# Performance work log

Measured on AMD Instinct MI355X. Metric: run time of the kernel, lower is better.

Reference implementation:

```python
import jax, jax.numpy as jnp
import numpy as np

EPS = 1e-12  # torch F.normalize eps

def _l2norm(t):
    # normalize over last axis (N), clamp norm like torch.nn.functional.normalize
    n = jnp.linalg.norm(t, axis=-1, keepdims=True)
    return t / jnp.maximum(n, EPS)

def setup_inputs() -> dict:
    key = jax.random.key(0)
    ks = jax.random.split(key, 4)
    B, N, D, H = 8, 4096, 768, 16
    x = jax.random.normal(ks[0], (B, N, D), dtype=jnp.float32)
    w_qkv = jax.random.normal(ks[1], (D, 3 * D), dtype=jnp.float32) * (D ** -0.5)
    temperature = jnp.ones((H, 1, 1), dtype=jnp.float32)
    w_proj = jax.random.normal(ks[2], (D, D), dtype=jnp.float32) * (D ** -0.5)
    b_proj = jnp.zeros((D,), dtype=jnp.float32)
    return {"x": x, "w_qkv": w_qkv, "temperature": temperature,
            "w_proj": w_proj, "b_proj": b_proj}

def reference(x, w_qkv, temperature, w_proj, b_proj):
    B, N, D = x.shape
    H = temperature.shape[0]
    C = D // H
    # qkv linear (no bias), split last dim as (3, H, C), move to (3, B, H, C, N)
    qkv = (x @ w_qkv).reshape(B, N, 3, H, C).transpose(2, 0, 3, 4, 1)
    q, k, v = qkv[0], qkv[1], qkv[2]            # each [B, H, C, N]
    q = _l2norm(q)
    k = _l2norm(k)
    # cross-covariance attention: small CxC matrix per head
    attn = jnp.einsum('bhcn,bhdn->bhcd', q, k) * temperature  # [B,H,C,C]
    attn = jax.nn.softmax(attn, axis=-1)
    out = jnp.einsum('bhcd,bhdn->bhcn', attn, v)  # [B,H,C,N]
    out = out.transpose(0, 3, 1, 2).reshape(B, N, D)  # B N (H C)
    return out @ w_proj + b_proj
```

## Files before the change

kernel.cpp:

```cpp
#include <hip/hip_runtime.h>
#include <stdint.h>

typedef __attribute__((ext_vector_type(4))) float          f32x4;
typedef __attribute__((ext_vector_type(8))) short          bf16x8;
typedef __attribute__((ext_vector_type(8))) unsigned short u16x8;
typedef __attribute__((ext_vector_type(4))) unsigned short u16x4;

static __device__ __forceinline__ unsigned short f2bf(float f){
  uint32_t u = __builtin_bit_cast(uint32_t, f);
  u += 0x7FFFu + ((u >> 16) & 1u);
  return (unsigned short)(u >> 16);
}
static __device__ __forceinline__ float bf2f(unsigned short h){
  uint32_t u = ((uint32_t)h) << 16;
  return __builtin_bit_cast(float, u);
}

static __device__ __forceinline__ uint32_t f2e4m3(float x){
  uint32_t u = __builtin_bit_cast(uint32_t, x);
  uint32_t s = (u >> 24) & 0x80u;
  uint32_t a = u & 0x7FFFFFFFu;
  if (a >= 0x43E00000u) return s | 0x7Eu;
  int ebits = (int)(a >> 23);
  uint32_t mfull = (a & 0x7FFFFFu) | 0x800000u;
  int shift = (ebits >= 121) ? 20 : 20 + (121 - ebits);
  if (shift > 31) return s;
  uint32_t q = mfull >> shift;
  uint32_t rem = mfull & ((1u << shift) - 1u);
  uint32_t half = 1u << (shift - 1);
  q += (rem > half || (rem == half && (q & 1u)));
  if (ebits >= 121){
    uint32_t E = (uint32_t)(ebits - 121 + 1);
    if (q == 16u){ E += 1u; q = 8u; }
    uint32_t man = q - 8u;
    if (E > 15u || (E == 15u && man == 7u)) return s | 0x7Eu;
    return s | (E << 3) | man;
  } else {
    if (q >= 8u) return s | (1u << 3) | (q - 8u);
    return s | q;
  }
}

static __device__ __forceinline__ uint32_t pk4_e4m3(float a0, float a1, float a2, float a3){
#if __has_builtin(__builtin_amdgcn_cvt_pk_fp8_f32)
  uint32_t pk = (uint32_t)__builtin_amdgcn_cvt_pk_fp8_f32(a0, a1, 0, false);
  pk = (uint32_t)__builtin_amdgcn_cvt_pk_fp8_f32(a2, a3, (int)pk, true);
  return pk;
#else
  return f2e4m3(a0) | (f2e4m3(a1) << 8) | (f2e4m3(a2) << 16) | (f2e4m3(a3) << 24);
#endif
}

#define GLL(SRC, DST) __builtin_amdgcn_global_load_lds(                         \
    (const __attribute__((address_space(1))) unsigned int*)(SRC),               \
    (__attribute__((address_space(3))) unsigned int*)(DST), 16, 0, 0)

__global__ void k_cvt(const float* __restrict__ in, unsigned short* __restrict__ out, long n){
  long i = ((long)blockIdx.x * blockDim.x + threadIdx.x) * 8;
  if (i >= n) return;
  const f32x4* p = (const f32x4*)(in + i);
  f32x4 a = p[0], b = p[1];
  u16x8 o;
  #pragma unroll
  for (int j = 0; j < 4; j++){ o[j] = f2bf(a[j]); o[4+j] = f2bf(b[j]); }
  *(u16x8*)(out + i) = o;
}

__global__ void k_tconv2(const float* __restrict__ wqkv, const float* __restrict__ wproj,
                         unsigned short* __restrict__ WT, unsigned short* __restrict__ WpT){
  __shared__ float tl[64][65];
  const int bx = blockIdx.x;
  const float* in = (bx < 24) ? wqkv : wproj;
  unsigned short* out = (bx < 24) ? WT : WpT;
  const int C = (bx < 24) ? 2304 : 768;
  const int c0 = ((bx < 24) ? bx : bx - 24) * 64, r0 = blockIdx.y * 64;
  const int t = threadIdx.x;
  {
    const int lr = t >> 2, lc = (t & 3) * 16;
    const f32x4* s = (const f32x4*)(in + (long)(r0 + lr) * C + c0 + lc);
    #pragma unroll
    for (int q = 0; q < 4; q++){
      f32x4 v = s[q];
      #pragma unroll
      for (int j = 0; j < 4; j++) tl[lr][lc + q*4 + j] = v[j];
    }
  }
  __syncthreads();
  {
    const int oc = t >> 2, orr = (t & 3) * 16;
    u16x8 o0, o1;
    #pragma unroll
    for (int i = 0; i < 8; i++){ o0[i] = f2bf(tl[orr + i][oc]); o1[i] = f2bf(tl[orr + 8 + i][oc]); }
    u16x8* dst = (u16x8*)(out + (long)(c0 + oc) * 768 + r0 + orr);
    dst[0] = o0; dst[1] = o1;
  }
}

__global__ void k_cvtwv(const float* __restrict__ w, unsigned short* __restrict__ out){
  const long idx = ((long)blockIdx.x * blockDim.x + threadIdx.x) * 8;
  const int e = (int)(idx / 768), hd = (int)(idx - (long)e * 768);
  const float* s = w + (long)e * 2304 + 1536 + hd;
  f32x4 a = *(const f32x4*)s, b = *(const f32x4*)(s + 4);
  u16x8 o;
  #pragma unroll
  for (int j = 0; j < 4; j++){ o[j] = f2bf(a[j]); o[4+j] = f2bf(b[j]); }
  *(u16x8*)(out + idx) = o;
}

static __device__ __forceinline__ bf16x8 ldfrag(const char* slot, int row, int ko){
  const int k2 = (ko ^ (row >> 1)) & 3;
  return *(const bf16x8*)(slot + row*64 + k2*16);
}

static __device__ __forceinline__ void stg256(const unsigned short* __restrict__ G, int row0, int ke,
                                              char* lds_slot, int t){
  #pragma unroll
  for (int l = 0; l < 2; l++){
    const int r  = l*128 + (t >> 2);
    const int k2 = (t & 3) ^ ((r >> 1) & 3);
    GLL((const char*)(G + (long)(row0 + r) * 768 + ke + k2 * 8),
        lds_slot + l*8192 + (t & 0x1C0) * 16);
  }
}

#define PHASE(BUF, KK, MH, STAGE_STMT, WAIT_STMT) do {                         \
    bf16x8 af[4];                                                              \
    if (MH == 0) {                                                             \
      _Pragma("unroll")                                                        \
      for (int ni = 0; ni < 4; ni++)                                           \
        bq[ni] = ldfrag(sB[BUF][KK], wn*64 + ni*16 + arow, ko);                \
    }                                                                          \
    _Pragma("unroll")                                                          \
    for (int mi = 0; mi < 4; mi++)                                             \
      af[mi] = ldfrag(sA[BUF][KK], wm*128 + MH*64 + mi*16 + arow, ko);         \
    __builtin_amdgcn_s_barrier();                                              \
    __builtin_amdgcn_s_setprio(1);                                             \
    _Pragma("unroll")                                                          \
    for (int mi = 0; mi < 4; mi++)                                             \
      _Pragma("unroll")                                                        \
      for (int ni = 0; ni < 4; ni++)                                           \
        acc[MH*4+mi][ni] = __builtin_amdgcn_mfma_f32_16x16x32_bf16(            \
            af[mi], bq[ni], acc[MH*4+mi][ni], 0, 0, 0);                        \
    __builtin_amdgcn_s_setprio(0);                                             \
    STAGE_STMT;                                                                \
    WAIT_STMT;                                                                 \
    __builtin_amdgcn_s_barrier();                                              \
  } while(0)

__global__ __launch_bounds__(512, 2)
void k_gemm256(const unsigned short* __restrict__ A, const unsigned short* __restrict__ BT,
               unsigned char* __restrict__ QT8, unsigned char* __restrict__ KT8,
               float* __restrict__ nrmp)
{
  __shared__ __attribute__((aligned(16))) char lds[131072];
  const int o  = blockIdx.x;
  const int wg = (o & 7) * 96 + (o >> 3);
  const int jt = wg % 6, mt = wg / 6;
  const int m0 = mt * 256, j0 = jt * 256;
  const int t = threadIdx.x, lane = t & 63, w = t >> 6;
  const int wm = w >> 2, wn = w & 3;
  const int arow = lane & 15, ko = lane >> 4;

  char* const sA[2][2] = {{lds,           lds + 16384},
                          {lds + 65536,   lds + 65536 + 16384}};
  char* const sB[2][2] = {{lds + 32768,   lds + 49152},
                          {lds + 65536 + 32768, lds + 65536 + 49152}};

  f32x4 acc[8][4] = {};

  stg256(BT, j0, 0,   sB[0][0], t);
  stg256(A,  m0, 0,   sA[0][0], t);
  stg256(BT, j0, 32,  sB[0][1], t);
  stg256(A,  m0, 32,  sA[0][1], t);
  stg256(BT, j0, 64,  sB[1][0], t);
  stg256(A,  m0, 64,  sA[1][0], t);
  stg256(BT, j0, 96,  sB[1][1], t);
  asm volatile("s_waitcnt vmcnt(6)" ::: "memory");
  __builtin_amdgcn_s_barrier();

  #pragma unroll 1
  for (int it = 0; it < 6; ++it){
    const int t1 = 2*it + 1, t2 = 2*it + 2, t3 = 2*it + 3;
    bf16x8 bq[4];
    PHASE(0,0,0, { stg256(A, m0, t1*64+32, sA[1][1], t); }, ;);
    PHASE(0,0,1, { if (t2 < 12) stg256(BT, j0, t2*64,    sB[0][0], t); }, ;);
    PHASE(0,1,0, { if (t2 < 12) stg256(A,  m0, t2*64,    sA[0][0], t); }, ;);
    PHASE(0,1,1, { if (t2 < 12) stg256(BT, j0, t2*64+32, sB[0][1], t); },
                 { if (it == 5) asm volatile("s_waitcnt vmcnt(0)" ::: "memory");
                   else         asm volatile("s_waitcnt vmcnt(6)" ::: "memory"); });
    PHASE(1,0,0, { if (t2 < 12) stg256(A,  m0, t2*64+32, sA[0][1], t); }, ;);
    PHASE(1,0,1, { if (t3 < 12) stg256(BT, j0, t3*64,    sB[1][0], t); }, ;);
    PHASE(1,1,0, { if (t3 < 12) stg256(A,  m0, t3*64,    sA[1][0], t); }, ;);
    PHASE(1,1,1, { if (t3 < 12) stg256(BT, j0, t3*64+32, sB[1][1], t); },
                 { if (it == 5) asm volatile("s_waitcnt vmcnt(0)" ::: "memory");
                   else         asm volatile("s_waitcnt vmcnt(6)" ::: "memory"); });
  }

  const int b = m0 >> 12;
  const int chunk = ((m0 & 4095) >> 7) + wm;
  #pragma unroll
  for (int ni = 0; ni < 4; ni++){
    float ss = 0.f;
    #pragma unroll
    for (int mi = 0; mi < 8; mi++)
      #pragma unroll
      for (int r = 0; r < 4; r++) ss += acc[mi][ni][r] * acc[mi][ni][r];
    ss += __shfl_xor(ss, 16);
    ss += __shfl_xor(ss, 32);
    if (lane < 16){
      const int jc = j0 + wn*64 + ni*16 + lane;
      const int s  = (jc >= 768);
      const int jl = jc - s * 768;
      const int h  = jl / 48;
      const int c  = jl - h * 48;
      nrmp[(long)(s*6144 + (b*16 + h)*48 + c)*32 + chunk] = ss;
    }
  }
  #pragma unroll
  for (int mi = 0; mi < 8; mi++){
    #pragma unroll
    for (int ni = 0; ni < 4; ni++){
      const int j  = wn*64 + ni*16 + (lane & 15);
      const int nl = wm*128 + mi*16 + (lane >> 4)*4;
      uint32_t pk = pk4_e4m3(acc[mi][ni][0], acc[mi][ni][1], acc[mi][ni][2], acc[mi][ni][3]);
      const int d = (nl >> 2) ^ ((j & 15) << 2);
      *(uint32_t*)(lds + (long)j*256 + (d << 2)) = pk;
    }
  }
  __syncthreads();
  for (int rr = 0; rr < 32; rr++){
    const int j  = w*32 + rr;
    const int jc = j0 + j;
    const int s  = (jc >= 768);
    const int jl = jc - s * 768;
    const int h  = jl / 48;
    const int c  = jl - h * 48;
    const int dp = lane ^ ((j & 15) << 2);
    uint32_t v = *(const uint32_t*)(lds + (long)j*256 + (dp << 2));
    *(uint32_t*)((s ? KT8 : QT8) + ((long)((b*16 + h)*48 + c) << 12) + (m0 & 4095) + lane*4) = v;
  }
}

static __device__ __forceinline__ void stageA512(const unsigned short* __restrict__ G, int row0, int ke,
                                                 char* slot, int t){
  const int r  = t >> 2;
  const int k2 = (t & 3) ^ ((r >> 1) & 3);
  GLL((const char*)(G + (long)(row0 + r) * 768 + ke + k2 * 8), slot + (t & 0x1C0) * 16);
}
static __device__ __forceinline__ void stageB512(const unsigned short* __restrict__ G, int row0, int ke,
                                                 char* slot, int t){
  #pragma unroll
  for (int l = 0; l < 2; l++){
    const int r  = l*128 + (t >> 2);
    const int k2 = (t & 3) ^ ((r >> 1) & 3);
    GLL((const char*)(G + (long)(row0 + r) * 768 + ke + k2 * 8), slot + l*8192 + (t & 0x1C0) * 16);
  }
}

#define VM0 asm volatile("s_waitcnt vmcnt(0)" ::: "memory")
#define VM3 asm volatile("s_waitcnt vmcnt(3)" ::: "memory")

#define PHASE1(CUR, STAGE_STMT, WAIT_STMT) do {                                \
    bf16x8 af[4], bq[4];                                                       \
    _Pragma("unroll")                                                          \
    for (int ni = 0; ni < 4; ni++)                                             \
      bq[ni] = ldfrag(sB[CUR], wn*64 + ni*16 + arow, ko);                      \
    _Pragma("unroll")                                                          \
    for (int mi = 0; mi < 4; mi++)                                             \
      af[mi] = ldfrag(sA[CUR], wm64 + mi*16 + arow, ko);                       \
    __builtin_amdgcn_s_barrier();                                              \
    __builtin_amdgcn_s_setprio(1);                                             \
    _Pragma("unroll")                                                          \
    for (int mi = 0; mi < 4; mi++)                                             \
      _Pragma("unroll")                                                        \
      for (int ni = 0; ni < 4; ni++)                                           \
        acc[mi][ni] = __builtin_amdgcn_mfma_f32_16x16x32_bf16(                 \
            af[mi], bq[ni], acc[mi][ni], 0, 0, 0);                             \
    __builtin_amdgcn_s_setprio(0);                                             \
    STAGE_STMT;                                                                \
    WAIT_STMT;                                                                 \
    __builtin_amdgcn_s_barrier();                                              \
  } while(0)

__global__ __launch_bounds__(512, 4)
void k_gemmP(const unsigned short* __restrict__ A, const unsigned short* __restrict__ BT,
             float* __restrict__ OUTF, const float* __restrict__ bias)
{
  __shared__ __attribute__((aligned(16))) char lds[73728];
  const int o  = blockIdx.x;
  const int wg = (o & 7) * 96 + (o >> 3);
  const int jt = wg % 3, mt = wg / 3;
  const int m0 = mt * 128, j0 = jt * 256;
  const int t = threadIdx.x, lane = t & 63, w = t >> 6;
  const int wm = w >> 2, wn = w & 3;
  const int wm64 = wm * 64;
  const int arow = lane & 15, ko = lane >> 4;
  const unsigned short* BTb = BT + ((long)(m0 >> 12)) * 589824;

  char* const sA[3] = {lds,          lds + 8192,          lds + 16384};
  char* const sB[3] = {lds + 24576,  lds + 24576 + 16384, lds + 24576 + 32768};

  f32x4 acc[4][4] = {};

  stageA512(A, m0, 0,  sA[0], t);  stageB512(BTb, j0, 0,  sB[0], t);
  stageA512(A, m0, 32, sA[1], t);  stageB512(BTb, j0, 32, sB[1], t);
  VM3;
  __builtin_amdgcn_s_barrier();

  #pragma unroll 1
  for (int g = 0; g < 7; ++g){
    const int kb = g * 96;
    PHASE1(0, { stageA512(A, m0, kb+64,  sA[2], t); stageB512(BTb, j0, kb+64,  sB[2], t); }, VM3);
    PHASE1(1, { stageA512(A, m0, kb+96,  sA[0], t); stageB512(BTb, j0, kb+96,  sB[0], t); }, VM3);
    PHASE1(2, { stageA512(A, m0, kb+128, sA[1], t); stageB512(BTb, j0, kb+128, sB[1], t); }, VM3);
  }
  PHASE1(0, { stageA512(A, m0, 736, sA[2], t); stageB512(BTb, j0, 736, sB[2], t); }, VM3);
  PHASE1(1, { ; }, VM0);
  PHASE1(2, { ; }, ;);

  #pragma unroll
  for (int mi = 0; mi < 4; mi++){
    #pragma unroll
    for (int ni = 0; ni < 4; ni++){
      const int jc = j0 + wn*64 + ni*16 + (lane & 15);
      const float bv = bias[jc];
      const long mr = (long)m0 + wm64 + mi*16 + (lane >> 4)*4;
      #pragma unroll
      for (int r = 0; r < 4; r++) OUTF[(mr + r) * 768 + jc] = acc[mi][ni][r] + bv;
    }
  }
}

__global__ __launch_bounds__(256)
void k_attn_part(const unsigned char* __restrict__ QT8, const unsigned char* __restrict__ KT8,
                 float* __restrict__ Spart)
{
  __shared__ float Sl[4][2304];
  const int bh = blockIdx.x, ksp = blockIdx.y;
  const int t = threadIdx.x, lane = t & 63, w = t >> 6;
  const unsigned char* qb = QT8 + ((long)bh * 48 << 12);
  const unsigned char* kb = KT8 + ((long)bh * 48 << 12);
  const int n00 = ksp * 1024 + w * 256;
  f32x4 acc[3][3] = {};
  for (int kt = 0; kt < 256; kt += 32){
    long af[3], bfr[3];
    #pragma unroll
    for (int ci = 0; ci < 3; ci++)
      af[ci]  = *(const long*)(qb + ((long)(ci*16 + (lane & 15)) << 12) + n00 + kt + (lane >> 4) * 8);
    #pragma unroll
    for (int di = 0; di < 3; di++)
      bfr[di] = *(const long*)(kb + ((long)(di*16 + (lane & 15)) << 12) + n00 + kt + (lane >> 4) * 8);
    #pragma unroll
    for (int ci = 0; ci < 3; ci++)
      #pragma unroll
      for (int di = 0; di < 3; di++)
        acc[ci][di] = __builtin_amdgcn_mfma_f32_16x16x32_fp8_fp8(af[ci], bfr[di], acc[ci][di], 0, 0, 0);
  }
  #pragma unroll
  for (int ci = 0; ci < 3; ci++)
    #pragma unroll
    for (int di = 0; di < 3; di++)
      #pragma unroll
      for (int r = 0; r < 4; r++)
        Sl[w][(ci*16 + (lane >> 4)*4 + r) * 48 + di*16 + (lane & 15)] = acc[ci][di][r];
  __syncthreads();
  float* outp = Spart + ((long)ksp * 128 + bh) * 2304;
  for (int idx = t; idx < 2304; idx += 256)
    outp[idx] = Sl[0][idx] + Sl[1][idx] + Sl[2][idx] + Sl[3][idx];
}

__global__ void k_softmax(const float* __restrict__ Spart, const float* __restrict__ nrmp,
                          const float* __restrict__ temp, unsigned short* __restrict__ attnT)
{
  __shared__ float invq[48], invk[48];
  const int bh = blockIdx.x, h = bh & 15;
  const int c = threadIdx.x;
  if (c < 48){
    float sq = 0.f, sk = 0.f;
    const float* pq = nrmp + (long)(bh*48 + c) * 32;
    const float* pk = nrmp + (long)(6144 + bh*48 + c) * 32;
    #pragma unroll
    for (int i = 0; i < 32; i++){ sq += pq[i]; sk += pk[i]; }
    invq[c] = 1.0f / fmaxf(sqrtf(sq), 1e-12f);
    invk[c] = 1.0f / fmaxf(sqrtf(sk), 1e-12f);
  }
  __syncthreads();
  if (c < 48){
    const float scq = invq[c] * temp[h];
    float row[48];
    #pragma unroll
    for (int d = 0; d < 48; d++){
      long base = ((long)bh * 48 + c) * 48 + d;
      float v = Spart[base] + Spart[base + 128L*2304] + Spart[base + 256L*2304] + Spart[base + 384L*2304];
      row[d] = v * scq * invk[d];
    }
    float mx = -1e30f;
    #pragma unroll
    for (int d = 0; d < 48; d++) mx = fmaxf(mx, row[d]);
    float s = 0.f;
    #pragma unroll
    for (int d = 0; d < 48; d++){ row[d] = expf(row[d] - mx); s += row[d]; }
    const float inv = 1.0f / s;
    unsigned short* ob = attnT + (long)bh * 48 * 64;
    #pragma unroll
    for (int d = 0; d < 48; d++) ob[d*64 + c] = f2bf(row[d] * inv);
    u16x8 z = {};
    *(u16x8*)(ob + c*64 + 48) = z;
    *(u16x8*)(ob + c*64 + 56) = z;
  }
}

__global__ __launch_bounds__(256)
void k_wmod2(const unsigned short* __restrict__ WpT, const unsigned short* __restrict__ attnT,
             unsigned short* __restrict__ WmodT)
{
  const int j0 = blockIdx.x * 256, h = blockIdx.y, b = blockIdx.z;
  const int t = threadIdx.x, lane = t & 63, w = t >> 6;
  const unsigned short* wp = WpT + h * 48;
  const unsigned short* ab = attnT + ((long)(b*16 + h)) * 48 * 64;
  f32x4 acc[4][3] = {};
  #pragma unroll
  for (int kt = 0; kt < 64; kt += 32){
    bf16x8 bfr[3];
    #pragma unroll
    for (int ni = 0; ni < 3; ni++)
      bfr[ni] = *(const bf16x8*)(ab + (ni*16 + (lane & 15))*64 + kt + (lane >> 4)*8);
    #pragma unroll
    for (int mi = 0; mi < 4; mi++){
      const int j = j0 + w*64 + mi*16 + (lane & 15);
      bf16x8 a = *(const bf16x8*)(wp + (long)j*768 + kt + (lane >> 4)*8);
      #pragma unroll
      for (int ni = 0; ni < 3; ni++)
        acc[mi][ni] = __builtin_amdgcn_mfma_f32_16x16x32_bf16(a, bfr[ni], acc[mi][ni], 0, 0, 0);
    }
  }
  #pragma unroll
  for (int mi = 0; mi < 4; mi++)
    #pragma unroll
    for (int ni = 0; ni < 3; ni++)
      #pragma unroll
      for (int r = 0; r < 4; r++){
        const int j = j0 + w*64 + mi*16 + (lane >> 4)*4 + r;
        const int d = ni*16 + (lane & 15);
        WmodT[(long)b*589824 + (long)j*768 + h*48 + d] = f2bf(acc[mi][ni][r]);
      }
}

__global__ __launch_bounds__(256)
void k_comb(const unsigned short* __restrict__ A, const unsigned short* __restrict__ BT,
            unsigned short* __restrict__ OUT)
{
  __shared__ unsigned short As[128 * 32];
  __shared__ unsigned short Bs[128 * 32];
  const int m0 = blockIdx.y * 128;
  const int j0 = blockIdx.x * 128;
  const int t = threadIdx.x;
  const int lane = t & 63;
  const int w = t >> 6, wm = w >> 1, wn = w & 1;

  f32x4 acc[4][4] = {};

  for (int kt = 0; kt < 768; kt += 32){
    if (kt) __syncthreads();
    #pragma unroll
    for (int i = 0; i < 2; i++){
      const char* ga = (const char*)A  + (long)(m0 + i*64 + (t >> 2)) * 1536 + kt*2 + (t & 3) * 16;
      const char* gb = (const char*)BT + (long)(j0 + i*64 + (t >> 2)) * 1536 + kt*2 + (t & 3) * 16;
      char* la = (char*)As + i*4096 + (t & 0xC0) * 16;
      char* lb = (char*)Bs + i*4096 + (t & 0xC0) * 16;
      GLL(ga, la);
      GLL(gb, lb);
    }
    __syncthreads();
    bf16x8 af[4], bfr[4];
    #pragma unroll
    for (int mi = 0; mi < 4; mi++)
      af[mi]  = *(const bf16x8*)&As[(wm*64 + mi*16 + (lane & 15)) * 32 + (lane >> 4) * 8];
    #pragma unroll
    for (int ni = 0; ni < 4; ni++)
      bfr[ni] = *(const bf16x8*)&Bs[(wn*64 + ni*16 + (lane & 15)) * 32 + (lane >> 4) * 8];
    #pragma unroll
    for (int mi = 0; mi < 4; mi++)
      #pragma unroll
      for (int ni = 0; ni < 4; ni++)
        acc[mi][ni] = __builtin_amdgcn_mfma_f32_16x16x32_bf16(af[mi], bfr[ni], acc[mi][ni], 0, 0, 0);
  }

  #pragma unroll
  for (int mi = 0; mi < 4; mi++)
    #pragma unroll
    for (int ni = 0; ni < 4; ni++){
      const int jc = j0 + wn*64 + ni*16 + (lane & 15);
      const long mr = (long)m0 + wm*64 + mi*16 + (lane >> 4) * 4;
      #pragma unroll
      for (int r = 0; r < 4; r++) OUT[(mr + r) * 768 + jc] = f2bf(acc[mi][ni][r]);
    }
}

extern "C" void kernel_launch(void* const* d_in, const int* in_sizes, int n_in,
                              void* d_out, int out_size, void* d_ws, size_t ws_size,
                              hipStream_t stream)
{
  (void)in_sizes; (void)n_in; (void)out_size; (void)ws_size;
  const float* x      = (const float*)d_in[0];
  const float* w_qkv  = (const float*)d_in[1];
  const float* temp   = (const float*)d_in[2];
  const float* w_proj = (const float*)d_in[3];
  const float* b_proj = (const float*)d_in[4];
  float* outF = (float*)d_out;

  char* ws = (char*)d_ws;
  size_t off = 0;
  auto alloc = [&](size_t bytes)->char*{ char* p = ws + off; off += (bytes + 255) & ~(size_t)255; return p; };

  unsigned short* x_bf  = (unsigned short*)alloc(50331648);
  unsigned short* WT    = (unsigned short*)alloc(2359296);
  unsigned short* WpT   = (unsigned short*)alloc(1179648);
  unsigned short* WvB   = (unsigned short*)alloc(1179648);
  unsigned char*  QT8   = (unsigned char*)alloc(50331648);
  unsigned char*  KT8   = QT8 + (long)6144 * 4096;
  float* nrmp           = (float*)alloc(12288L * 32 * 4);
  float* Spart          = (float*)alloc(4L * 128 * 2304 * 4);
  unsigned short* attnT = (unsigned short*)alloc(786432);
  unsigned short* WmodT = (unsigned short*)alloc(9437184);
  unsigned short* WcombT= (unsigned short*)alloc(9437184);

  k_cvt<<<12288, 256, 0, stream>>>(x, x_bf, 25165824L);
  k_tconv2<<<dim3(36, 12), 256, 0, stream>>>(w_qkv, w_proj, WT, WpT);
  k_cvtwv<<<288, 256, 0, stream>>>(w_qkv, WvB);
  k_gemm256<<<768, 512, 0, stream>>>(x_bf, WT, QT8, KT8, nrmp);
  k_attn_part<<<dim3(128, 4), 256, 0, stream>>>(QT8, KT8, Spart);
  k_softmax<<<128, 64, 0, stream>>>(Spart, nrmp, temp, attnT);
  k_wmod2<<<dim3(3, 16, 8), 256, 0, stream>>>(WpT, attnT, WmodT);
  k_comb<<<dim3(6, 48), 256, 0, stream>>>(WmodT, WvB, WcombT);
  k_gemmP<<<768, 512, 0, stream>>>(x_bf, WcombT, outF, b_proj);
}
```

Baseline: 222.8 us.

## Compute QK projection GEMM in FP8 and fuse preprocessing kernels into one launch

The Q/K projection GEMM now reads x and the transposed QK weights as FP8 e4m3 and uses fp8 MFMA instructions, halving operand bytes and K-loop iterations. The three conversion kernels are merged into one launch that also writes an FP8 copy of x alongside the bf16 copy. This cuts GEMM load traffic and launch count, but adds an extra 25 MB write in preprocessing and lowers the precision of Q and K before normalization.

```diff
diff --git a/kernel.cpp b/kernel.cpp
--- a/kernel.cpp
+++ b/kernel.cpp
@@ -5,6 +5,7 @@
 typedef __attribute__((ext_vector_type(8))) short          bf16x8;
 typedef __attribute__((ext_vector_type(8))) unsigned short u16x8;
 typedef __attribute__((ext_vector_type(4))) unsigned short u16x4;
+typedef __attribute__((ext_vector_type(2))) long           longx2;
 
 static __device__ __forceinline__ unsigned short f2bf(float f){
   uint32_t u = __builtin_bit_cast(uint32_t, f);
@@ -40,7 +41,6 @@
     return s | q;
   }
 }
-
 static __device__ __forceinline__ uint32_t pk4_e4m3(float a0, float a1, float a2, float a3){
 #if __has_builtin(__builtin_amdgcn_cvt_pk_fp8_f32)
   uint32_t pk = (uint32_t)__builtin_amdgcn_cvt_pk_fp8_f32(a0, a1, 0, false);
@@ -55,92 +55,114 @@
     (const __attribute__((address_space(1))) unsigned int*)(SRC),               \
     (__attribute__((address_space(3))) unsigned int*)(DST), 16, 0, 0)
 
-__global__ void k_cvt(const float* __restrict__ in, unsigned short* __restrict__ out, long n){
-  long i = ((long)blockIdx.x * blockDim.x + threadIdx.x) * 8;
-  if (i >= n) return;
-  const f32x4* p = (const f32x4*)(in + i);
-  f32x4 a = p[0], b = p[1];
-  u16x8 o;
-  #pragma unroll
-  for (int j = 0; j < 4; j++){ o[j] = f2bf(a[j]); o[4+j] = f2bf(b[j]); }
-  *(u16x8*)(out + i) = o;
-}
-
-__global__ void k_tconv2(const float* __restrict__ wqkv, const float* __restrict__ wproj,
-                         unsigned short* __restrict__ WT, unsigned short* __restrict__ WpT){
+__global__ void k_pre(const float* __restrict__ x, const float* __restrict__ wqkv,
+                      const float* __restrict__ wproj,
+                      unsigned short* __restrict__ xbf, unsigned char* __restrict__ x8,
+                      unsigned char* __restrict__ WT8, unsigned short* __restrict__ WpT,
+                      unsigned short* __restrict__ WvB)
+{
   __shared__ float tl[64][65];
-  const int bx = blockIdx.x;
-  const float* in = (bx < 24) ? wqkv : wproj;
-  unsigned short* out = (bx < 24) ? WT : WpT;
-  const int C = (bx < 24) ? 2304 : 768;
-  const int c0 = ((bx < 24) ? bx : bx - 24) * 64, r0 = blockIdx.y * 64;
-  const int t = threadIdx.x;
-  {
-    const int lr = t >> 2, lc = (t & 3) * 16;
-    const f32x4* s = (const f32x4*)(in + (long)(r0 + lr) * C + c0 + lc);
-    #pragma unroll
-    for (int q = 0; q < 4; q++){
-      f32x4 v = s[q];
-      #pragma unroll
-      for (int j = 0; j < 4; j++) tl[lr][lc + q*4 + j] = v[j];
-    }
-  }
-  __syncthreads();
-  {
-    const int oc = t >> 2, orr = (t & 3) * 16;
-    u16x8 o0, o1;
-    #pragma unroll
-    for (int i = 0; i < 8; i++){ o0[i] = f2bf(tl[orr + i][oc]); o1[i] = f2bf(tl[orr + 8 + i][oc]); }
-    u16x8* dst = (u16x8*)(out + (long)(c0 + oc) * 768 + r0 + orr);
-    dst[0] = o0; dst[1] = o1;
-  }
-}
-
-__global__ void k_cvtwv(const float* __restrict__ w, unsigned short* __restrict__ out){
-  const long idx = ((long)blockIdx.x * blockDim.x + threadIdx.x) * 8;
-  const int e = (int)(idx / 768), hd = (int)(idx - (long)e * 768);
-  const float* s = w + (long)e * 2304 + 1536 + hd;
-  f32x4 a = *(const f32x4*)s, b = *(const f32x4*)(s + 4);
-  u16x8 o;
-  #pragma unroll
-  for (int j = 0; j < 4; j++){ o[j] = f2bf(a[j]); o[4+j] = f2bf(b[j]); }
-  *(u16x8*)(out + idx) = o;
+  const int bx = blockIdx.x, t = threadIdx.x;
+  if (bx < 12288){
+    const long i = ((long)bx * 256 + t) * 8;
+    const f32x4* p = (const f32x4*)(x + i);
+    f32x4 a = p[0], b = p[1];
+    u16x8 o;
+    #pragma unroll
+    for (int j = 0; j < 4; j++){ o[j] = f2bf(a[j]); o[4+j] = f2bf(b[j]); }
+    *(u16x8*)(xbf + i) = o;
+    uint32_t p0 = pk4_e4m3(a[0], a[1], a[2], a[3]);
+    uint32_t p1 = pk4_e4m3(b[0], b[1], b[2], b[3]);
+    *(uint32_t*)(x8 + i)     = p0;
+    *(uint32_t*)(x8 + i + 4) = p1;
+  } else if (bx < 12720){
+    const int idx = bx - 12288;
+    const int cb = idx % 36, rb = idx / 36;
+    const int qk = (cb < 24);
+    const float* in = qk ? wqkv : wproj;
+    const int C = qk ? 2304 : 768;
+    const int c0 = (qk ? cb : cb - 24) * 64, r0 = rb * 64;
+    {
+      const int lr = t >> 2, lc = (t & 3) * 16;
+      const f32x4* s = (const f32x4*)(in + (long)(r0 + lr) * C + c0 + lc);
+      #pragma unroll
+      for (int q = 0; q < 4; q++){
+        f32x4 v = s[q];
+        #pragma unroll
+        for (int j = 0; j < 4; j++) tl[lr][lc + q*4 + j] = v[j];
+      }
+    }
+    __syncthreads();
+    {
+      const int oc = t >> 2, orr = (t & 3) * 16;
+      if (qk){
+        uint32_t w0 = pk4_e4m3(tl[orr+0][oc],  tl[orr+1][oc],  tl[orr+2][oc],  tl[orr+3][oc]);
+        uint32_t w1 = pk4_e4m3(tl[orr+4][oc],  tl[orr+5][oc],  tl[orr+6][oc],  tl[orr+7][oc]);
+        uint32_t w2 = pk4_e4m3(tl[orr+8][oc],  tl[orr+9][oc],  tl[orr+10][oc], tl[orr+11][oc]);
+        uint32_t w3 = pk4_e4m3(tl[orr+12][oc], tl[orr+13][oc], tl[orr+14][oc], tl[orr+15][oc]);
+        uint32_t* d = (uint32_t*)(WT8 + (long)(c0 + oc) * 768 + r0 + orr);
+        d[0] = w0; d[1] = w1; d[2] = w2; d[3] = w3;
+      } else {
+        u16x8 o0, o1;
+        #pragma unroll
+        for (int i = 0; i < 8; i++){ o0[i] = f2bf(tl[orr + i][oc]); o1[i] = f2bf(tl[orr + 8 + i][oc]); }
+        u16x8* dst = (u16x8*)(WpT + (long)(c0 + oc) * 768 + r0 + orr);
+        dst[0] = o0; dst[1] = o1;
+      }
+    }
+  } else {
+    const long idx = ((long)(bx - 12720) * 256 + t) * 8;
+    const int e = (int)(idx / 768), hd = (int)(idx - (long)e * 768);
+    const float* s = wqkv + (long)e * 2304 + 1536 + hd;
+    f32x4 a = *(const f32x4*)s, b = *(const f32x4*)(s + 4);
+    u16x8 o;
+    #pragma unroll
+    for (int j = 0; j < 4; j++){ o[j] = f2bf(a[j]); o[4+j] = f2bf(b[j]); }
+    *(u16x8*)(WvB + idx) = o;
+  }
 }
 
 static __device__ __forceinline__ bf16x8 ldfrag(const char* slot, int row, int ko){
   const int k2 = (ko ^ (row >> 1)) & 3;
   return *(const bf16x8*)(slot + row*64 + k2*16);
 }
-
-static __device__ __forceinline__ void stg256(const unsigned short* __restrict__ G, int row0, int ke,
-                                              char* lds_slot, int t){
+static __device__ __forceinline__ longx2 ldfrag8(const char* slot, int row, int ko){
+  const int k2 = (ko ^ (row >> 1)) & 3;
+  return *(const longx2*)(slot + row*64 + k2*16);
+}
+
+static __device__ __forceinline__ void stg8(const unsigned char* __restrict__ G, int row0, int keB,
+                                            char* lds_slot, int t){
   #pragma unroll
   for (int l = 0; l < 2; l++){
-    const int r  = l*128 + (t >> 2);
-    const int k2 = (t & 3) ^ ((r >> 1) & 3);
-    GLL((const char*)(G + (long)(row0 + r) * 768 + ke + k2 * 8),
+    const int r = l*128 + (t >> 2);
+    const int c = (t & 3) ^ ((r >> 1) & 3);
+    GLL((const char*)(G + (long)(row0 + r) * 768 + keB + c * 16),
         lds_slot + l*8192 + (t & 0x1C0) * 16);
   }
 }
 
-#define PHASE(BUF, KK, MH, STAGE_STMT, WAIT_STMT) do {                         \
-    bf16x8 af[4];                                                              \
+#define PH8(BUF, KK, MH, STAGE_STMT, WAIT_STMT) do {                           \
+    longx2 af[4];                                                              \
     if (MH == 0) {                                                             \
       _Pragma("unroll")                                                        \
       for (int ni = 0; ni < 4; ni++)                                           \
-        bq[ni] = ldfrag(sB[BUF][KK], wn*64 + ni*16 + arow, ko);                \
+        bq[ni] = ldfrag8(sB[BUF][KK], wn*64 + ni*16 + arow, ko);               \
     }                                                                          \
     _Pragma("unroll")                                                          \
     for (int mi = 0; mi < 4; mi++)                                             \
-      af[mi] = ldfrag(sA[BUF][KK], wm*128 + MH*64 + mi*16 + arow, ko);         \
+      af[mi] = ldfrag8(sA[BUF][KK], wm*128 + MH*64 + mi*16 + arow, ko);        \
     __builtin_amdgcn_s_barrier();                                              \
     __builtin_amdgcn_s_setprio(1);                                             \
     _Pragma("unroll")                                                          \
     for (int mi = 0; mi < 4; mi++)                                             \
       _Pragma("unroll")                                                        \
-      for (int ni = 0; ni < 4; ni++)                                           \
-        acc[MH*4+mi][ni] = __builtin_amdgcn_mfma_f32_16x16x32_bf16(            \
-            af[mi], bq[ni], acc[MH*4+mi][ni], 0, 0, 0);                        \
+      for (int ni = 0; ni < 4; ni++){                                          \
+        acc[MH*4+mi][ni] = __builtin_amdgcn_mfma_f32_16x16x32_fp8_fp8(         \
+            af[mi][0], bq[ni][0], acc[MH*4+mi][ni], 0, 0, 0);                  \
+        acc[MH*4+mi][ni] = __builtin_amdgcn_mfma_f32_16x16x32_fp8_fp8(         \
+            af[mi][1], bq[ni][1], acc[MH*4+mi][ni], 0, 0, 0);                  \
+      }                                                                        \
     __builtin_amdgcn_s_setprio(0);                                             \
     STAGE_STMT;                                                                \
     WAIT_STMT;                                                                 \
@@ -148,7 +170,7 @@
   } while(0)
 
 __global__ __launch_bounds__(512, 2)
-void k_gemm256(const unsigned short* __restrict__ A, const unsigned short* __restrict__ BT,
+void k_gemm256(const unsigned char* __restrict__ A8, const unsigned char* __restrict__ BT8,
                unsigned char* __restrict__ QT8, unsigned char* __restrict__ KT8,
                float* __restrict__ nrmp)
 {
@@ -168,32 +190,32 @@
 
   f32x4 acc[8][4] = {};
 
-  stg256(BT, j0, 0,   sB[0][0], t);
-  stg256(A,  m0, 0,   sA[0][0], t);
-  stg256(BT, j0, 32,  sB[0][1], t);
-  stg256(A,  m0, 32,  sA[0][1], t);
-  stg256(BT, j0, 64,  sB[1][0], t);
-  stg256(A,  m0, 64,  sA[1][0], t);
-  stg256(BT, j0, 96,  sB[1][1], t);
+  stg8(BT8, j0, 0,   sB[0][0], t);
+  stg8(A8,  m0, 0,   sA[0][0], t);
+  stg8(BT8, j0, 64,  sB[0][1], t);
+  stg8(A8,  m0, 64,  sA[0][1], t);
+  stg8(BT8, j0, 128, sB[1][0], t);
+  stg8(A8,  m0, 128, sA[1][0], t);
+  stg8(BT8, j0, 192, sB[1][1], t);
   asm volatile("s_waitcnt vmcnt(6)" ::: "memory");
   __builtin_amdgcn_s_barrier();
 
   #pragma unroll 1
-  for (int it = 0; it < 6; ++it){
+  for (int it = 0; it < 3; ++it){
     const int t1 = 2*it + 1, t2 = 2*it + 2, t3 = 2*it + 3;
-    bf16x8 bq[4];
-    PHASE(0,0,0, { stg256(A, m0, t1*64+32, sA[1][1], t); }, ;);
-    PHASE(0,0,1, { if (t2 < 12) stg256(BT, j0, t2*64,    sB[0][0], t); }, ;);
-    PHASE(0,1,0, { if (t2 < 12) stg256(A,  m0, t2*64,    sA[0][0], t); }, ;);
-    PHASE(0,1,1, { if (t2 < 12) stg256(BT, j0, t2*64+32, sB[0][1], t); },
-                 { if (it == 5) asm volatile("s_waitcnt vmcnt(0)" ::: "memory");
-                   else         asm volatile("s_waitcnt vmcnt(6)" ::: "memory"); });
-    PHASE(1,0,0, { if (t2 < 12) stg256(A,  m0, t2*64+32, sA[0][1], t); }, ;);
-    PHASE(1,0,1, { if (t3 < 12) stg256(BT, j0, t3*64,    sB[1][0], t); }, ;);
-    PHASE(1,1,0, { if (t3 < 12) stg256(A,  m0, t3*64,    sA[1][0], t); }, ;);
-    PHASE(1,1,1, { if (t3 < 12) stg256(BT, j0, t3*64+32, sB[1][1], t); },
-                 { if (it == 5) asm volatile("s_waitcnt vmcnt(0)" ::: "memory");
-                   else         asm volatile("s_waitcnt vmcnt(6)" ::: "memory"); });
+    longx2 bq[4];
+    PH8(0,0,0, { stg8(A8, m0, t1*128+64, sA[1][1], t); }, ;);
+    PH8(0,0,1, { if (t2 < 6) stg8(BT8, j0, t2*128,    sB[0][0], t); }, ;);
+    PH8(0,1,0, { if (t2 < 6) stg8(A8,  m0, t2*128,    sA[0][0], t); }, ;);
+    PH8(0,1,1, { if (t2 < 6) stg8(BT8, j0, t2*128+64, sB[0][1], t); },
+               { if (it == 2) asm volatile("s_waitcnt vmcnt(0)" ::: "memory");
+                 else         asm volatile("s_waitcnt vmcnt(6)" ::: "memory"); });
+    PH8(1,0,0, { if (t2 < 6) stg8(A8,  m0, t2*128+64, sA[0][1], t); }, ;);
+    PH8(1,0,1, { if (t3 < 6) stg8(BT8, j0, t3*128,    sB[1][0], t); }, ;);
+    PH8(1,1,0, { if (t3 < 6) stg8(A8,  m0, t3*128,    sA[1][0], t); }, ;);
+    PH8(1,1,1, { if (t3 < 6) stg8(BT8, j0, t3*128+64, sB[1][1], t); },
+               { if (it == 2) asm volatile("s_waitcnt vmcnt(0)" ::: "memory");
+                 else         asm volatile("s_waitcnt vmcnt(6)" ::: "memory"); });
   }
 
   const int b = m0 >> 12;
@@ -514,7 +536,8 @@
   auto alloc = [&](size_t bytes)->char*{ char* p = ws + off; off += (bytes + 255) & ~(size_t)255; return p; };
 
   unsigned short* x_bf  = (unsigned short*)alloc(50331648);
-  unsigned short* WT    = (unsigned short*)alloc(2359296);
+  unsigned char*  x8    = (unsigned char*)alloc(25165824);
+  unsigned char*  WT8   = (unsigned char*)alloc(1179648);
   unsigned short* WpT   = (unsigned short*)alloc(1179648);
   unsigned short* WvB   = (unsigned short*)alloc(1179648);
   unsigned char*  QT8   = (unsigned char*)alloc(50331648);
@@ -525,10 +548,8 @@
   unsigned short* WmodT = (unsigned short*)alloc(9437184);
   unsigned short* WcombT= (unsigned short*)alloc(9437184);
 
-  k_cvt<<<12288, 256, 0, stream>>>(x, x_bf, 25165824L);
-  k_tconv2<<<dim3(36, 12), 256, 0, stream>>>(w_qkv, w_proj, WT, WpT);
-  k_cvtwv<<<288, 256, 0, stream>>>(w_qkv, WvB);
-  k_gemm256<<<768, 512, 0, stream>>>(x_bf, WT, QT8, KT8, nrmp);
+  k_pre<<<13008, 256, 0, stream>>>(x, w_qkv, w_proj, x_bf, x8, WT8, WpT, WvB);
+  k_gemm256<<<768, 512, 0, stream>>>(x8, WT8, QT8, KT8, nrmp);
   k_attn_part<<<dim3(128, 4), 256, 0, stream>>>(QT8, KT8, Spart);
   k_softmax<<<128, 64, 0, stream>>>(Spart, nrmp, temp, attnT);
   k_wmod2<<<dim3(3, 16, 8), 256, 0, stream>>>(WpT, attnT, WmodT);
```

Result: faster. 211.0 us (-5.3%).
